# Performance work log

Hardware: AMD Instinct MI355X
Metric: run time of the kernel (lower is better)

Reference implementation:

```python
import jax, jax.numpy as jnp
import numpy as np

B, S, D, H = 128, 256, 256, 8   # graphs, nodes/graph, dim_h, heads
N = B * S
E = 524288
DH = D // H
BN_EPS = 1e-5

def _bn(v, g, b):
    # BatchNorm1d forward with batch statistics (biased var), eval-dropout model
    m = v.mean(0)
    var = v.var(0)
    return (v - m) * jax.lax.rsqrt(var + BN_EPS) * g + b

def setup_inputs() -> dict:
    key = jax.random.key(0)
    ks = jax.random.split(key, 40)
    x = jax.random.normal(ks[0], (N, D), jnp.float32)
    src = jax.random.randint(ks[1], (E,), 0, N)
    dst = (src // S) * S + jax.random.randint(ks[2], (E,), 0, S)  # intra-graph edges
    edge_index = jnp.stack([src, dst]).astype(jnp.int64)
    def lin(k, i, o):
        return (jax.random.normal(k, (i, o), jnp.float32) / np.float32(np.sqrt(i)))
    inp = {
        'x': x, 'edge_index': edge_index,
        'W_gcn': lin(ks[3], D, D), 'b_gcn': jnp.zeros((D,), jnp.float32),
        'W_gin1': lin(ks[4], D, D), 'b_gin1': jnp.zeros((D,), jnp.float32),
        'W_gin2': lin(ks[5], D, D), 'b_gin2': jnp.zeros((D,), jnp.float32),
        'g_kv': jnp.ones((D,), jnp.float32), 'be_kv': jnp.zeros((D,), jnp.float32),
        'Wq1': lin(ks[6], D, D), 'bq1': jnp.zeros((D,), jnp.float32),
        'Wq2': lin(ks[7], D, D), 'bq2': jnp.zeros((D,), jnp.float32),
        'Wq_a': lin(ks[8], D, D), 'bq_a': jnp.zeros((D,), jnp.float32),
        'Wk_a': lin(ks[9], D, D), 'bk_a': jnp.zeros((D,), jnp.float32),
        'Wv_a': lin(ks[10], D, D), 'bv_a': jnp.zeros((D,), jnp.float32),
        'Wo_a': lin(ks[11], D, D), 'bo_a': jnp.zeros((D,), jnp.float32),
        'g_attn': jnp.ones((D,), jnp.float32), 'be_attn': jnp.zeros((D,), jnp.float32),
        'Wf1': lin(ks[12], D, 2 * D), 'bf1': jnp.zeros((2 * D,), jnp.float32),
        'Wf2': lin(ks[13], 2 * D, D), 'bf2': jnp.zeros((D,), jnp.float32),
        'g2': jnp.ones((D,), jnp.float32), 'be2': jnp.zeros((D,), jnp.float32),
    }
    return inp

def _forward(x, edge_index,
             W_gcn, b_gcn, W_gin1, b_gin1, W_gin2, b_gin2, g_kv, be_kv,
             Wq1, bq1, Wq2, bq2,
             Wq_a, bq_a, Wk_a, bk_a, Wv_a, bv_a, Wo_a, bo_a, g_attn, be_attn,
             Wf1, bf1, Wf2, bf2, g2, be2):
    row, col = edge_index[0], edge_index[1]
    h_in1 = x

    # ---- expert 0: GCNConv (add self loops + symmetric norm) ----
    loops = jnp.arange(N, dtype=row.dtype)
    row2 = jnp.concatenate([row, loops])
    col2 = jnp.concatenate([col, loops])
    deg = jax.ops.segment_sum(jnp.ones_like(row2, jnp.float32), col2, num_segments=N)
    dinv = jnp.where(deg > 0, jax.lax.rsqrt(deg), 0.0)
    norm = dinv[row2] * dinv[col2]                     # [E+N]
    xw = x @ W_gcn                                      # [N, D]
    h_gcn = jax.ops.segment_sum(norm[:, None] * xw[row2], col2, num_segments=N) + b_gcn
    e0 = _bn(h_gcn, g_kv, be_kv)

    # ---- expert 1: GINConv (eps=0, sum aggregation, 2-layer MLP) ----
    agg = jax.ops.segment_sum(x[row], col, num_segments=N)
    h_gin = jax.nn.relu((x + agg) @ W_gin1 + b_gin1) @ W_gin2 + b_gin2
    e1 = _bn(h_gin, g_kv, be_kv)

    # ---- global expert normalization (torch .std -> unbiased) ----
    allo = jnp.concatenate([e0, e1], axis=0)
    gm = allo.mean()
    gs = jnp.std(allo, ddof=1)
    e0 = (e0 - gm) / (gs + 1e-8)
    e1 = (e1 - gm) / (gs + 1e-8)

    # ---- uniform routing & kv residual mix ----
    kv = 0.5 * e0 + 0.5 * e1 + 0.1 * h_in1              # [N, D]

    # ---- dense batching (equal-sized graphs -> pure reshape, full mask) ----
    q_dense = h_in1.reshape(B, S, D)
    kv_dense = kv.reshape(B, S, D)

    # ---- q projection MLP ----
    q_dense = jax.nn.relu(q_dense @ Wq1 + bq1) @ Wq2 + bq2

    # ---- multihead attention (batch_first, no padding) ----
    qh = (q_dense @ Wq_a + bq_a).reshape(B, S, H, DH)
    kh = (kv_dense @ Wk_a + bk_a).reshape(B, S, H, DH)
    vh = (kv_dense @ Wv_a + bv_a).reshape(B, S, H, DH)
    scores = jnp.einsum('bqhd,bkhd->bhqk', qh, kh) / np.float32(np.sqrt(DH))
    attn = jax.nn.softmax(scores, axis=-1)
    o = jnp.einsum('bhqk,bkhd->bqhd', attn, vh).reshape(B, S, D)
    h_attn = (o @ Wo_a + bo_a).reshape(N, D)

    # ---- residual + norm + FFN block ----
    h = _bn(h_in1 + h_attn, g_attn, be_attn)
    h_ff = jax.nn.relu(h @ Wf1 + bf1) @ Wf2 + bf2
    h = _bn(h + h_ff, g2, be2)
    return h

def reference(x, edge_index,
              W_gcn, b_gcn, W_gin1, b_gin1, W_gin2, b_gin2, g_kv, be_kv,
              Wq1, bq1, Wq2, bq2,
              Wq_a, bq_a, Wk_a, bk_a, Wv_a, bv_a, Wo_a, bo_a, g_attn, be_attn,
              Wf1, bf1, Wf2, bf2, g2, be2):
    return _forward(x, edge_index,
                    W_gcn, b_gcn, W_gin1, b_gin1, W_gin2, b_gin2, g_kv, be_kv,
                    Wq1, bq1, Wq2, bq2,
                    Wq_a, bq_a, Wk_a, bk_a, Wv_a, bv_a, Wo_a, bo_a, g_attn, be_attn,
                    Wf1, bf1, Wf2, bf2, g2, be2)
```

## Files before the change

kernel.cpp:

```cpp
#include <hip/hip_runtime.h>
#include <hip/hip_bf16.h>

typedef __hip_bfloat16 bf16;
typedef __attribute__((ext_vector_type(8))) short short8;
typedef __attribute__((ext_vector_type(4))) short short4v;
typedef __attribute__((ext_vector_type(4))) float f32x4;
typedef __attribute__((ext_vector_type(4))) int i32x4;

#define N_ 32768
#define D_ 256
#define S_ 256
#define B_ 128
#define E_ 524288

static __device__ __forceinline__ f32x4 mfma16(short8 a, short8 b, f32x4 c) {
  return __builtin_amdgcn_mfma_f32_16x16x32_bf16(a, b, c, 0, 0, 0);
}
static __device__ __forceinline__ f32x4 fzero4() {
  f32x4 z; z[0] = 0.f; z[1] = 0.f; z[2] = 0.f; z[3] = 0.f; return z;
}
static __device__ __forceinline__ float bits2f(short s) {
  unsigned u = ((unsigned)(unsigned short)s) << 16;
  return __builtin_bit_cast(float, u);
}
static __device__ __forceinline__ short f2bits(float f) {
  bf16 b = __float2bfloat16(f);
  return __builtin_bit_cast(short, b);
}
static __device__ __forceinline__ float tof(float x) { return x; }
static __device__ __forceinline__ float tof(bf16 x) { return __bfloat162float(x); }

#define GLOAD_LDS16(G, L) __builtin_amdgcn_global_load_lds( \
    (const __attribute__((address_space(1))) void*)(G),     \
    (__attribute__((address_space(3))) void*)(L), 16, 0, 0)

template<int F>
__global__ __launch_bounds__(256)
void gemm_bt(const bf16* __restrict__ A, const bf16* __restrict__ Bt,
             const float* __restrict__ bias, const void* __restrict__ resid,
             float* __restrict__ Cf, bf16* __restrict__ Cb,
             float* __restrict__ Sp, float* __restrict__ SSp,
             int M, int Nc, int K, long bsA, long bsB, long bsC)
{
  __shared__ __align__(16) bf16 lA[128 * 32];
  __shared__ __align__(16) bf16 lB[128 * 32];
  __shared__ float sS[2][128], sSS[2][128];
  const int z = blockIdx.z;
  const bf16* Ab = A + (long)z * bsA;
  const bf16* Bb = Bt + (long)z * bsB;
  const int m0 = blockIdx.x * 128, n0 = blockIdx.y * 128;
  const int tid = threadIdx.x;
  const int lane = tid & 63;
  const int w = tid >> 6, wr = w >> 1, wc = w & 1;
  const int g = lane >> 4, r = lane & 15, ko = g * 8;
  const int srow = lane >> 2, skw = (lane & 3) * 8;

  f32x4 acc[4][4];
  for (int i = 0; i < 4; i++) for (int j = 0; j < 4; j++) acc[i][j] = fzero4();

  for (int k0 = 0; k0 < K; k0 += 32) {
    __syncthreads();
    for (int i = 0; i < 2; i++) {
      const int c = w * 2 + i;
      GLOAD_LDS16(Ab + (long)(m0 + c * 16 + srow) * K + k0 + skw, lA + c * 512);
      GLOAD_LDS16(Bb + (long)(n0 + c * 16 + srow) * K + k0 + skw, lB + c * 512);
    }
    __syncthreads();
    short8 af[4], bfv[4];
    for (int mi = 0; mi < 4; mi++)
      af[mi] = *(const short8*)&lA[(wr * 64 + mi * 16 + r) * 32 + ko];
    for (int ni = 0; ni < 4; ni++)
      bfv[ni] = *(const short8*)&lB[(wc * 64 + ni * 16 + r) * 32 + ko];
    for (int mi = 0; mi < 4; mi++)
      for (int ni = 0; ni < 4; ni++)
        acc[mi][ni] = mfma16(af[mi], bfv[ni], acc[mi][ni]);
  }

  float cs[4] = {0, 0, 0, 0}, css[4] = {0, 0, 0, 0};
  for (int mi = 0; mi < 4; mi++) for (int ni = 0; ni < 4; ni++) {
    const int row = m0 + wr * 64 + mi * 16 + g * 4;
    const int col = n0 + wc * 64 + ni * 16 + r;
    float bv = (F & 2) ? bias[col] : 0.0f;
    for (int j = 0; j < 4; j++) {
      long idx = (long)(row + j) * Nc + col;
      float v = acc[mi][ni][j] + bv;
      if (F & 4)  v += ((const float*)resid)[(long)z * bsC + idx];
      if (F & 64) v += bits2f(((const short*)resid)[(long)z * bsC + idx]);
      if (F & 1)  v = fmaxf(v, 0.0f);
      if (F & 32) { cs[ni] += v; css[ni] += v * v; }
      if (F & 8)  Cf[(long)z * bsC + idx] = v;
      if (F & 16) Cb[(long)z * bsC + idx] = __float2bfloat16(v);
    }
  }
  if (F & 32) {
    for (int ni = 0; ni < 4; ni++) {
      cs[ni]  += __shfl_xor(cs[ni], 16);  cs[ni]  += __shfl_xor(cs[ni], 32);
      css[ni] += __shfl_xor(css[ni], 16); css[ni] += __shfl_xor(css[ni], 32);
    }
    if (lane < 16) {
      for (int ni = 0; ni < 4; ni++) {
        sS[wr][wc * 64 + ni * 16 + lane]  = cs[ni];
        sSS[wr][wc * 64 + ni * 16 + lane] = css[ni];
      }
    }
    __syncthreads();
    if (tid < 128) {
      atomicAdd(&Sp[n0 + tid],  sS[0][tid] + sS[1][tid]);
      atomicAdd(&SSp[n0 + tid], sSS[0][tid] + sSS[1][tid]);
    }
  }
}

__global__ __launch_bounds__(256, 2)
void attn_k(const bf16* __restrict__ qh, const bf16* __restrict__ kh,
            const bf16* __restrict__ vh, bf16* __restrict__ ob)
{
  const int h = blockIdx.x, b = blockIdx.y;
  const int tid = threadIdx.x, lane = tid & 63, w = tid >> 6;
  const int g = lane >> 4, r = lane & 15, ko = g * 8;
  __shared__ __align__(16) bf16 lK[256 * 32];
  __shared__ __align__(16) bf16 lV[32 * 256];
  char* lKc = (char*)lK;
  char* lVc = (char*)lV;

  for (int i = 0; i < 4; i++) {
    int c = tid + i * 256;
    int row = c >> 2, p4 = c & 3;
    short8 v = *(const short8*)(kh + (long)(b * 256 + row) * 256 + h * 32 + p4 * 8);
    *(short8*)(lKc + ((row * 64 + p4 * 16) ^ ((row & 7) << 4))) = v;
  }
  for (int i = 0; i < 4; i++) {
    int c = tid + i * 256;
    int s = c >> 2, part = c & 3;
    short8 v = *(const short8*)(vh + (long)(b * 256 + s) * 256 + h * 32 + part * 8);
    for (int j = 0; j < 8; j++) {
      int dh = part * 8 + j;
      int sw = ((dh & 7) ^ ((dh >> 3) << 1)) & 7;
      *(short*)(lVc + ((dh * 512 + s * 2) ^ (sw << 4))) = v[j];
    }
  }
  __syncthreads();

  const float scale = 0.17677669529663687f;
  const int idx0 = (((lane >> 4) & 1) * 32 + r) * 4;
  const int idx1 = idx0 + 64;
  const bool selhi = lane >= 32;

  for (int mc = 0; mc < 4; mc++) {
    const long qbase = (long)b * 256 + w * 64 + mc * 16;
    short8 qf = *(const short8*)(qh + (qbase + r) * 256 + h * 32 + ko);
    f32x4 sc[16];
    #pragma unroll
    for (int nc = 0; nc < 16; nc++) {
      int row = nc * 16 + r;
      short8 kf = *(const short8*)(lKc + ((row * 64 + g * 16) ^ ((r & 7) << 4)));
      sc[nc] = mfma16(kf, qf, fzero4());
    }
    f32x4 m4 = sc[0];
    #pragma unroll
    for (int nc = 1; nc < 16; nc++)
      for (int j = 0; j < 4; j++) m4[j] = fmaxf(m4[j], sc[nc][j]);
    float mx = fmaxf(fmaxf(m4[0], m4[1]), fmaxf(m4[2], m4[3]));
    mx = fmaxf(mx, __shfl_xor(mx, 16));
    mx = fmaxf(mx, __shfl_xor(mx, 32));
    f32x4 s4 = fzero4();
    #pragma unroll
    for (int nc = 0; nc < 16; nc++)
      for (int j = 0; j < 4; j++) {
        float p = __expf((sc[nc][j] - mx) * scale);
        sc[nc][j] = p; s4[j] += p;
      }
    float sum = s4[0] + s4[1] + s4[2] + s4[3];
    sum += __shfl_xor(sum, 16);
    sum += __shfl_xor(sum, 32);
    const float invs = 1.0f / sum;
    f32x4 oa[2]; oa[0] = fzero4(); oa[1] = fzero4();
    #pragma unroll
    for (int kc = 0; kc < 8; kc++) {
      int pkA0, pkA1, pkB0, pkB1;
      {
        const f32x4 pa = sc[2 * kc], pb = sc[2 * kc + 1];
        unsigned a0 = (unsigned short)f2bits(pa[0] * invs);
        unsigned a1 = (unsigned short)f2bits(pa[1] * invs);
        unsigned a2 = (unsigned short)f2bits(pa[2] * invs);
        unsigned a3 = (unsigned short)f2bits(pa[3] * invs);
        unsigned b0 = (unsigned short)f2bits(pb[0] * invs);
        unsigned b1 = (unsigned short)f2bits(pb[1] * invs);
        unsigned b2 = (unsigned short)f2bits(pb[2] * invs);
        unsigned b3 = (unsigned short)f2bits(pb[3] * invs);
        pkA0 = (int)((a1 << 16) | a0);
        pkA1 = (int)((a3 << 16) | a2);
        pkB0 = (int)((b1 << 16) | b0);
        pkB1 = (int)((b3 << 16) | b2);
      }
      int A0 = __builtin_amdgcn_ds_bpermute(idx0, pkA0);
      int A1 = __builtin_amdgcn_ds_bpermute(idx0, pkA1);
      int B0 = __builtin_amdgcn_ds_bpermute(idx0, pkB0);
      int B1 = __builtin_amdgcn_ds_bpermute(idx0, pkB1);
      int C0 = __builtin_amdgcn_ds_bpermute(idx1, pkA0);
      int C1 = __builtin_amdgcn_ds_bpermute(idx1, pkA1);
      int D0 = __builtin_amdgcn_ds_bpermute(idx1, pkB0);
      int D1 = __builtin_amdgcn_ds_bpermute(idx1, pkB1);
      i32x4 av;
      av[0] = selhi ? B0 : A0;
      av[1] = selhi ? B1 : A1;
      av[2] = selhi ? D0 : C0;
      av[3] = selhi ? D1 : C1;
      short8 af = __builtin_bit_cast(short8, av);
      #pragma unroll
      for (int n = 0; n < 2; n++) {
        int dh = n * 16 + r;
        int sw = ((dh & 7) ^ ((dh >> 3) << 1)) & 7;
        short8 bv = *(const short8*)(lVc + ((dh * 512 + kc * 64 + g * 16) ^ (sw << 4)));
        oa[n] = mfma16(af, bv, oa[n]);
      }
    }
    #pragma unroll
    for (int n = 0; n < 2; n++)
      for (int j = 0; j < 4; j++)
        ob[(qbase + g * 4 + j) * 256 + h * 32 + n * 16 + r] =
          __float2bfloat16(oa[n][j]);
  }
}

template<typename TIN>
__global__ __launch_bounds__(256)
void transpose_cast_k(const TIN* __restrict__ in, bf16* __restrict__ out,
                      int in_rs, int out_rs, long zhi, long out_zs)
{
  __shared__ float tile[32][33];
  const int z = blockIdx.z;
  const long ioff = (long)z * zhi;
  const long ooff = (long)z * out_zs;
  const int tx = threadIdx.x, ty = threadIdx.y;
  const int c = blockIdx.x * 32 + tx;
  const int rb = blockIdx.y * 32;
  for (int i = 0; i < 4; i++)
    tile[ty + i * 8][tx] = tof(in[ioff + (long)(rb + ty + i * 8) * in_rs + c]);
  __syncthreads();
  const int oc = rb + tx;
  const int orb = blockIdx.x * 32;
  for (int i = 0; i < 4; i++)
    out[ooff + (long)(orb + ty + i * 8) * out_rs + oc] =
      __float2bfloat16(tile[tx][ty + i * 8]);
}

__global__ __launch_bounds__(256)
void w9t_k(const float* w0, const float* w1, const float* w2, const float* w3,
           const float* w4, const float* w5, const float* w6, const float* w7,
           const float* w8, bf16* __restrict__ out)
{
  __shared__ float tile[32][33];
  const float* srcs[9] = {w0, w1, w2, w3, w4, w5, w6, w7, w8};
  const int wi = blockIdx.z;
  const float* in = srcs[wi];
  bf16* o = out + (long)wi * 65536;
  const int tx = threadIdx.x, ty = threadIdx.y;
  const int c = blockIdx.x * 32 + tx;
  const int rb = blockIdx.y * 32;
  for (int i = 0; i < 4; i++)
    tile[ty + i * 8][tx] = in[(rb + ty + i * 8) * 256 + c];
  __syncthreads();
  const int oc = rb + tx;
  const int orb = blockIdx.x * 32;
  for (int i = 0; i < 4; i++)
    o[(orb + ty + i * 8) * 256 + oc] = __float2bfloat16(tile[tx][ty + i * 8]);
}

__global__ __launch_bounds__(256)
void cast4_k(const float* __restrict__ in, bf16* __restrict__ out)
{
  long i = ((long)blockIdx.x * 256 + threadIdx.x) * 4;
  float4 v = *(const float4*)(in + i);
  short4v o;
  o[0] = f2bits(v.x); o[1] = f2bits(v.y); o[2] = f2bits(v.z); o[3] = f2bits(v.w);
  *(short4v*)(out + i) = o;
}

__global__ __launch_bounds__(256)
void edge_cnt_k(const int* __restrict__ ei, unsigned* __restrict__ cnt)
{
  int e = blockIdx.x * 256 + threadIdx.x;
  int src = ei[e], dst = ei[E_ + e];
  long idx = ((long)(src >> 8) * 256 + (dst & 255)) * 256 + (src & 255);
  atomicAdd(&cnt[idx >> 1], 1u << ((idx & 1) * 16));
}

__global__ __launch_bounds__(256)
void deg_k(const unsigned* __restrict__ cnt, float* __restrict__ dinv)
{
  int rid = blockIdx.x * 16 + (threadIdx.x >> 4);
  int l16 = threadIdx.x & 15;
  const uint4* rp = (const uint4*)(cnt + (long)rid * 128);
  unsigned s = 0;
  for (int i = 0; i < 2; i++) {
    uint4 v = rp[l16 + i * 16];
    s += (v.x & 0xFFFF) + (v.x >> 16) + (v.y & 0xFFFF) + (v.y >> 16)
       + (v.z & 0xFFFF) + (v.z >> 16) + (v.w & 0xFFFF) + (v.w >> 16);
  }
  s += __shfl_xor(s, 1); s += __shfl_xor(s, 2);
  s += __shfl_xor(s, 4); s += __shfl_xor(s, 8);
  if (l16 == 0) dinv[rid] = rsqrtf((float)s + 1.0f);
}

__global__ __launch_bounds__(256)
void adj_derive_k(const unsigned* __restrict__ cnt, const float* __restrict__ dinv,
                  bf16* __restrict__ gin, bf16* __restrict__ gcn)
{
  long i = ((long)blockIdx.x * 256 + threadIdx.x) * 4;
  uint2 cp = *(const uint2*)(cnt + (i >> 1));
  float cv[4] = {(float)(cp.x & 0xFFFF), (float)(cp.x >> 16),
                 (float)(cp.y & 0xFFFF), (float)(cp.y >> 16)};
  long row = i >> 8;
  int g = (int)(row >> 8), dst = (int)(row & 255);
  int src0 = (int)(i & 255);
  float dd = dinv[row];
  const float* ds = dinv + (long)g * 256 + src0;
  short4v oi, oc;
  for (int j = 0; j < 4; j++) {
    float gv = cv[j] * dd * ds[j];
    if (src0 + j == dst) gv += dd * dd;
    oi[j] = f2bits(cv[j]);
    oc[j] = f2bits(gv);
  }
  *(short4v*)(gin + i) = oi;
  *(short4v*)(gcn + i) = oc;
}

__global__ __launch_bounds__(256)
void expert_stats_k(const float* __restrict__ S0, const float* __restrict__ SS0,
                    const float* __restrict__ S1, const float* __restrict__ SS1,
                    const float* __restrict__ gkv, const float* __restrict__ bkv,
                    float* __restrict__ kA, float* __restrict__ kB,
                    float* __restrict__ kC)
{
  const int d = threadIdx.x;
  const float invN = 1.0f / 32768.0f;
  float m0 = S0[d] * invN, v0 = SS0[d] * invN - m0 * m0;
  float a0 = gkv[d] * rsqrtf(v0 + 1e-5f), c0 = bkv[d] - m0 * a0;
  float m1 = S1[d] * invN, v1 = SS1[d] * invN - m1 * m1;
  float a1 = gkv[d] * rsqrtf(v1 + 1e-5f), c1 = bkv[d] - m1 * a1;
  float gsum = a0 * S0[d] + 32768.0f * c0 + a1 * S1[d] + 32768.0f * c1;
  float gss  = a0 * a0 * SS0[d] + 2.0f * a0 * c0 * S0[d] + 32768.0f * c0 * c0
             + a1 * a1 * SS1[d] + 2.0f * a1 * c1 * S1[d] + 32768.0f * c1 * c1;
  __shared__ float r1[256], r2[256];
  r1[d] = gsum; r2[d] = gss;
  __syncthreads();
  for (int s = 128; s > 0; s >>= 1) {
    if (d < s) { r1[d] += r1[d + s]; r2[d] += r2[d + s]; }
    __syncthreads();
  }
  const float cntall = 16777216.0f;
  float tg = r1[0], tss = r2[0];
  float gm = tg / cntall;
  float var = (tss - tg * tg / cntall) / (cntall - 1.0f);
  float gs = sqrtf(fmaxf(var, 0.f)) + 1e-8f;
  kA[d] = 0.5f * a0 / gs;
  kB[d] = 0.5f * a1 / gs;
  kC[d] = 0.5f * (c0 + c1 - 2.0f * gm) / gs;
}

__global__ __launch_bounds__(256)
void kv_mix_k(const bf16* __restrict__ hgcn, const bf16* __restrict__ hgin,
              const bf16* __restrict__ xb, const float* __restrict__ kA,
              const float* __restrict__ kB, const float* __restrict__ kC,
              bf16* __restrict__ kv)
{
  long i = ((long)blockIdx.x * 256 + threadIdx.x) * 8;
  int d0 = (int)(i & 255);
  short8 a = *(const short8*)(hgcn + i);
  short8 b = *(const short8*)(hgin + i);
  short8 c = *(const short8*)(xb + i);
  short8 o;
  for (int j = 0; j < 8; j++) {
    int d = d0 + j;
    float v = kA[d] * bits2f(a[j]) + kB[d] * bits2f(b[j]) + kC[d] + 0.1f * bits2f(c[j]);
    o[j] = f2bits(v);
  }
  *(short8*)(kv + i) = o;
}

template<int MODE>
__global__ __launch_bounds__(256)
void bn_apply_k(const bf16* __restrict__ in, const float* __restrict__ S,
                const float* __restrict__ SSq, const float* __restrict__ gg,
                const float* __restrict__ bb, float* __restrict__ outf,
                bf16* __restrict__ outb)
{
  long i = ((long)blockIdx.x * 256 + threadIdx.x) * 8;
  int d0 = (int)(i & 255);
  short8 v = *(const short8*)(in + i);
  const float invN = 1.0f / 32768.0f;
  float4 o0, o1; short8 o8;
  for (int j = 0; j < 8; j++) {
    int d = d0 + j;
    float m = S[d] * invN;
    float var = SSq[d] * invN - m * m;
    float a = gg[d] * rsqrtf(var + 1e-5f);
    float c = bb[d] - m * a;
    float o = a * bits2f(v[j]) + c;
    if (MODE & 1) { if (j < 4) (&o0.x)[j] = o; else (&o1.x)[j - 4] = o; }
    if (MODE & 2) o8[j] = f2bits(o);
  }
  if (MODE & 1) { *(float4*)(outf + i) = o0; *(float4*)(outf + i + 4) = o1; }
  if (MODE & 2) *(short8*)(outb + i) = o8;
}

static constexpr size_t OFF_S0 = 0, OFF_SS0 = 1024, OFF_S1 = 2048, OFF_SS1 = 3072;
static constexpr size_t OFF_S2 = 4096, OFF_SS2 = 5120, OFF_S3 = 6144, OFF_SS3 = 7168;
static constexpr size_t OFF_KA = 8192, OFF_KB = 9216, OFF_KC = 10240;
static constexpr size_t OFF_CNT = 16384;
static constexpr size_t CNT_BYTES = (size_t)B_ * S_ * S_ * 2;
static constexpr size_t ZERO_BYTES = OFF_CNT + CNT_BYTES;
static constexpr size_t OFF_DINV = ZERO_BYTES;
static constexpr size_t OFF_W = OFF_DINV + 131072;
static constexpr size_t NDB2 = (size_t)N_ * D_ * 2;
static constexpr size_t OFF_ADJGINB = OFF_W + 1703936;
static constexpr size_t OFF_ADJGCNB = OFF_ADJGINB + NDB2;
static constexpr size_t OFF_XB   = OFF_ADJGCNB + NDB2;
static constexpr size_t OFF_XT   = OFF_XB + NDB2;
static constexpr size_t OFF_AGG  = OFF_XT + NDB2;
static constexpr size_t OFF_GIN  = OFF_AGG + NDB2;
static constexpr size_t OFF_KV   = OFF_GIN + NDB2;
static constexpr size_t OFF_HGCN = OFF_KV + NDB2;
static constexpr size_t OFF_HGIN = OFF_HGCN + NDB2;

extern "C" void kernel_launch(void* const* d_in, const int* in_sizes, int n_in,
                              void* d_out, int out_size, void* d_ws, size_t ws_size,
                              hipStream_t stream)
{
  (void)in_sizes; (void)n_in; (void)out_size; (void)ws_size;
  const float* x      = (const float*)d_in[0];
  const int*   ei     = (const int*)d_in[1];
  const float* W_gcn  = (const float*)d_in[2];
  const float* b_gcn  = (const float*)d_in[3];
  const float* W_gin1 = (const float*)d_in[4];
  const float* b_gin1 = (const float*)d_in[5];
  const float* W_gin2 = (const float*)d_in[6];
  const float* b_gin2 = (const float*)d_in[7];
  const float* g_kv   = (const float*)d_in[8];
  const float* be_kv  = (const float*)d_in[9];
  const float* Wq1    = (const float*)d_in[10];
  const float* bq1    = (const float*)d_in[11];
  const float* Wq2    = (const float*)d_in[12];
  const float* bq2    = (const float*)d_in[13];
  const float* Wq_a   = (const float*)d_in[14];
  const float* bq_a   = (const float*)d_in[15];
  const float* Wk_a   = (const float*)d_in[16];
  const float* bk_a   = (const float*)d_in[17];
  const float* Wv_a   = (const float*)d_in[18];
  const float* bv_a   = (const float*)d_in[19];
  const float* Wo_a   = (const float*)d_in[20];
  const float* bo_a   = (const float*)d_in[21];
  const float* g_attn = (const float*)d_in[22];
  const float* be_attn= (const float*)d_in[23];
  const float* Wf1    = (const float*)d_in[24];
  const float* bf1    = (const float*)d_in[25];
  const float* Wf2    = (const float*)d_in[26];
  const float* bf2    = (const float*)d_in[27];
  const float* g2     = (const float*)d_in[28];
  const float* be2    = (const float*)d_in[29];

  char* ws = (char*)d_ws;
  float* S0  = (float*)(ws + OFF_S0);  float* SS0 = (float*)(ws + OFF_SS0);
  float* S1  = (float*)(ws + OFF_S1);  float* SS1 = (float*)(ws + OFF_SS1);
  float* S2  = (float*)(ws + OFF_S2);  float* SS2 = (float*)(ws + OFF_SS2);
  float* S3  = (float*)(ws + OFF_S3);  float* SS3 = (float*)(ws + OFF_SS3);
  float* kA  = (float*)(ws + OFF_KA);  float* kB  = (float*)(ws + OFF_KB);
  float* kC  = (float*)(ws + OFF_KC);
  unsigned* cntA = (unsigned*)(ws + OFF_CNT);
  float* dinv = (float*)(ws + OFF_DINV);
  bf16* wT = (bf16*)(ws + OFF_W);
  bf16 *WgcnT = wT,            *Wgin1T = wT + 65536,  *Wgin2T = wT + 131072;
  bf16 *Wq1T  = wT + 196608,   *Wq2T   = wT + 262144, *WqaT   = wT + 327680;
  bf16 *WkaT  = wT + 393216,   *WvaT   = wT + 458752, *WoaT   = wT + 524288;
  bf16 *Wf1T  = wT + 589824,   *Wf2T   = wT + 720896;
  bf16* adjGINb = (bf16*)(ws + OFF_ADJGINB);
  bf16* adjGCNb = (bf16*)(ws + OFF_ADJGCNB);
  bf16* xb    = (bf16*)(ws + OFF_XB);
  bf16* xT    = (bf16*)(ws + OFF_XT);
  bf16* aggb  = (bf16*)(ws + OFF_AGG);
  bf16* gin_in= (bf16*)(ws + OFF_GIN);
  bf16* kv_bf = (bf16*)(ws + OFF_KV);
  bf16* hgcnb = (bf16*)(ws + OFF_HGCN);
  bf16* hginb = (bf16*)(ws + OFF_HGIN);
  bf16* gin_h  = adjGCNb;
  bf16* qhb    = adjGINb;
  bf16* q1b    = xT;
  bf16* qb     = aggb;
  bf16* khb    = gin_in;
  bf16* vhb    = hgcnb;
  bf16* ob     = hginb;
  bf16* tbufb  = (bf16*)(ws + OFF_CNT);
  bf16* hb     = xb;
  bf16* f1b    = adjGINb;
  bf16* t2b    = gin_in;
  float* outp  = (float*)d_out;

  hipMemsetAsync(d_ws, 0, ZERO_BYTES, stream);

  dim3 tb(32, 8);
  w9t_k<<<dim3(8, 8, 9), tb, 0, stream>>>(W_gcn, W_gin1, W_gin2, Wq1, Wq2,
                                          Wq_a, Wk_a, Wv_a, Wo_a, wT);
  transpose_cast_k<float><<<dim3(16, 8, 1), tb, 0, stream>>>(Wf1, Wf1T, 512, 256, 0, 0);
  transpose_cast_k<float><<<dim3(8, 16, 1), tb, 0, stream>>>(Wf2, Wf2T, 256, 512, 0, 0);
  cast4_k<<<8192, 256, 0, stream>>>(x, xb);
  transpose_cast_k<float><<<dim3(8, 8, 128), tb, 0, stream>>>(x, xT, 256, 256, 65536, 65536);
  edge_cnt_k<<<2048, 256, 0, stream>>>(ei, cntA);
  deg_k<<<2048, 256, 0, stream>>>(cntA, dinv);
  adj_derive_k<<<8192, 256, 0, stream>>>(cntA, dinv, adjGINb, adjGCNb);
  gemm_bt<16><<<dim3(2, 2, 128), 256, 0, stream>>>(adjGCNb, xT, nullptr, nullptr,
      nullptr, aggb, nullptr, nullptr, 256, 256, 256, 65536, 65536, 65536);
  gemm_bt<80><<<dim3(2, 2, 128), 256, 0, stream>>>(adjGINb, xT, nullptr, xb,
      nullptr, gin_in, nullptr, nullptr, 256, 256, 256, 65536, 65536, 65536);
  gemm_bt<50><<<dim3(256, 2, 1), 256, 0, stream>>>(aggb, WgcnT, b_gcn, nullptr,
      nullptr, hgcnb, S0, SS0, N_, 256, 256, 0, 0, 0);
  gemm_bt<19><<<dim3(256, 2, 1), 256, 0, stream>>>(gin_in, Wgin1T, b_gin1, nullptr,
      nullptr, gin_h, nullptr, nullptr, N_, 256, 256, 0, 0, 0);
  gemm_bt<50><<<dim3(256, 2, 1), 256, 0, stream>>>(gin_h, Wgin2T, b_gin2, nullptr,
      nullptr, hginb, S1, SS1, N_, 256, 256, 0, 0, 0);
  expert_stats_k<<<1, 256, 0, stream>>>(S0, SS0, S1, SS1, g_kv, be_kv, kA, kB, kC);
  kv_mix_k<<<4096, 256, 0, stream>>>(hgcnb, hginb, xb, kA, kB, kC, kv_bf);
  gemm_bt<19><<<dim3(256, 2, 1), 256, 0, stream>>>(xb, Wq1T, bq1, nullptr,
      nullptr, q1b, nullptr, nullptr, N_, 256, 256, 0, 0, 0);
  gemm_bt<18><<<dim3(256, 2, 1), 256, 0, stream>>>(q1b, Wq2T, bq2, nullptr,
      nullptr, qb, nullptr, nullptr, N_, 256, 256, 0, 0, 0);
  gemm_bt<18><<<dim3(256, 2, 1), 256, 0, stream>>>(qb, WqaT, bq_a, nullptr,
      nullptr, qhb, nullptr, nullptr, N_, 256, 256, 0, 0, 0);
  gemm_bt<18><<<dim3(256, 2, 1), 256, 0, stream>>>(kv_bf, WkaT, bk_a, nullptr,
      nullptr, khb, nullptr, nullptr, N_, 256, 256, 0, 0, 0);
  gemm_bt<18><<<dim3(256, 2, 1), 256, 0, stream>>>(kv_bf, WvaT, bv_a, nullptr,
      nullptr, vhb, nullptr, nullptr, N_, 256, 256, 0, 0, 0);
  attn_k<<<dim3(8, 128), 256, 0, stream>>>(qhb, khb, vhb, ob);
  gemm_bt<114><<<dim3(256, 2, 1), 256, 0, stream>>>(ob, WoaT, bo_a, xb,
      nullptr, tbufb, S2, SS2, N_, 256, 256, 0, 0, 0);
  bn_apply_k<2><<<4096, 256, 0, stream>>>(tbufb, S2, SS2, g_attn, be_attn, nullptr, hb);
  gemm_bt<19><<<dim3(256, 4, 1), 256, 0, stream>>>(hb, Wf1T, bf1, nullptr,
      nullptr, f1b, nullptr, nullptr, N_, 512, 256, 0, 0, 0);
  gemm_bt<114><<<dim3(256, 2, 1), 256, 0, stream>>>(f1b, Wf2T, bf2, hb,
      nullptr, t2b, S3, SS3, N_, 256, 512, 0, 0, 0);
  bn_apply_k<1><<<4096, 256, 0, stream>>>(t2b, S3, SS3, g2, be2, outp, nullptr);
}
```

Measured before the change: 342.9 us.

## Fuse chained GIN and query linear layers into LDS-resident MLP kernel, merge K/V GEMM

Adds a kernel that runs 2 or 3 chained 256x256 linear layers per 64-row tile, keeping intermediate activations in swizzled LDS. It replaces the separate GIN two-layer GEMMs and the three-stage query projection chain, removing intermediate global writes and reads and several launches. The K and V projections become one 512-wide GEMM with a second bias pointer, and the attention kernel reads them with a 512 stride. It also raises wave priority around the attention MFMA loops. The cost is that the fused kernel reloads full weight tiles per block with a simple, unpipelined K loop and has smaller per-wave tiles.

```diff
diff --git a/kernel.cpp b/kernel.cpp
--- a/kernel.cpp
+++ b/kernel.cpp
@@ -37,7 +37,8 @@
 template<int F>
 __global__ __launch_bounds__(256)
 void gemm_bt(const bf16* __restrict__ A, const bf16* __restrict__ Bt,
-             const float* __restrict__ bias, const void* __restrict__ resid,
+             const float* __restrict__ bias, const float* __restrict__ biasB,
+             const void* __restrict__ resid,
              float* __restrict__ Cf, bf16* __restrict__ Cb,
              float* __restrict__ Sp, float* __restrict__ SSp,
              int M, int Nc, int K, long bsA, long bsB, long bsC)
@@ -80,7 +81,11 @@
   for (int mi = 0; mi < 4; mi++) for (int ni = 0; ni < 4; ni++) {
     const int row = m0 + wr * 64 + mi * 16 + g * 4;
     const int col = n0 + wc * 64 + ni * 16 + r;
-    float bv = (F & 2) ? bias[col] : 0.0f;
+    float bv = 0.0f;
+    if (F & 2) {
+      if ((F & 128) && col >= 256) bv = biasB[col - 256];
+      else bv = bias[col];
+    }
     for (int j = 0; j < 4; j++) {
       long idx = (long)(row + j) * Nc + col;
       float v = acc[mi][ni][j] + bv;
@@ -111,9 +116,132 @@
   }
 }
 
+template<int STAGES, bool STATS>
+__global__ __launch_bounds__(512)
+void mlp_fused(const bf16* __restrict__ A,
+               const bf16* __restrict__ B1, const float* __restrict__ b1,
+               const bf16* __restrict__ B2, const float* __restrict__ b2,
+               const bf16* __restrict__ B3, const float* __restrict__ b3,
+               bf16* __restrict__ C, float* __restrict__ Sp, float* __restrict__ SSp)
+{
+  __shared__ __align__(16) bf16 lA[64 * 32];
+  __shared__ __align__(16) bf16 lB[256 * 32];
+  __shared__ __align__(16) bf16 lC[64 * 256];
+  char* lCc = (char*)lC;
+  const int tid = threadIdx.x;
+  const int lane = tid & 63;
+  const int w = tid >> 6;
+  const int mh = w >> 2, nq = w & 3;
+  const int g = lane >> 4, r = lane & 15, ko = g * 8;
+  const int m0 = blockIdx.x * 64;
+
+  f32x4 acc[2][4];
+  for (int i = 0; i < 2; i++) for (int j = 0; j < 4; j++) acc[i][j] = fzero4();
+
+  for (int k0 = 0; k0 < 256; k0 += 32) {
+    __syncthreads();
+    if (tid < 256)
+      GLOAD_LDS16(A + (long)(m0 + (tid >> 2)) * 256 + k0 + (tid & 3) * 8,
+                  lA + w * 512);
+    GLOAD_LDS16(B1 + (long)(tid >> 2) * 256 + k0 + (tid & 3) * 8,
+                lB + w * 512);
+    GLOAD_LDS16(B1 + (long)((tid + 512) >> 2) * 256 + k0 + ((tid + 512) & 3) * 8,
+                lB + w * 512 + 4096);
+    __syncthreads();
+    short8 af[2], bfv[4];
+    for (int mi = 0; mi < 2; mi++)
+      af[mi] = *(const short8*)&lA[(mh * 32 + mi * 16 + r) * 32 + ko];
+    for (int ni = 0; ni < 4; ni++)
+      bfv[ni] = *(const short8*)&lB[(nq * 64 + ni * 16 + r) * 32 + ko];
+    for (int mi = 0; mi < 2; mi++)
+      for (int ni = 0; ni < 4; ni++)
+        acc[mi][ni] = mfma16(af[mi], bfv[ni], acc[mi][ni]);
+  }
+  for (int mi = 0; mi < 2; mi++) for (int ni = 0; ni < 4; ni++) {
+    const int col = nq * 64 + ni * 16 + r;
+    const float bv = b1[col];
+    for (int j = 0; j < 4; j++) {
+      const int row = mh * 32 + mi * 16 + g * 4 + j;
+      float v = fmaxf(acc[mi][ni][j] + bv, 0.0f);
+      *(short*)(lCc + ((row * 512 + col * 2) ^ ((row & 7) << 4))) = f2bits(v);
+    }
+  }
+  __syncthreads();
+
+  const bf16* Bs = B2;
+  for (int s = 1; s < STAGES; s++) {
+    for (int i = 0; i < 2; i++) for (int j = 0; j < 4; j++) acc[i][j] = fzero4();
+    for (int k0 = 0; k0 < 256; k0 += 32) {
+      __syncthreads();
+      GLOAD_LDS16(Bs + (long)(tid >> 2) * 256 + k0 + (tid & 3) * 8,
+                  lB + w * 512);
+      GLOAD_LDS16(Bs + (long)((tid + 512) >> 2) * 256 + k0 + ((tid + 512) & 3) * 8,
+                  lB + w * 512 + 4096);
+      __syncthreads();
+      short8 af[2], bfv[4];
+      for (int mi = 0; mi < 2; mi++) {
+        const int row = mh * 32 + mi * 16 + r;
+        af[mi] = *(const short8*)(lCc +
+                  ((row * 512 + (k0 + ko) * 2) ^ ((row & 7) << 4)));
+      }
+      for (int ni = 0; ni < 4; ni++)
+        bfv[ni] = *(const short8*)&lB[(nq * 64 + ni * 16 + r) * 32 + ko];
+      for (int mi = 0; mi < 2; mi++)
+        for (int ni = 0; ni < 4; ni++)
+          acc[mi][ni] = mfma16(af[mi], bfv[ni], acc[mi][ni]);
+    }
+    if (s < STAGES - 1) {
+      __syncthreads();
+      for (int mi = 0; mi < 2; mi++) for (int ni = 0; ni < 4; ni++) {
+        const int col = nq * 64 + ni * 16 + r;
+        const float bv = b2[col];
+        for (int j = 0; j < 4; j++) {
+          const int row = mh * 32 + mi * 16 + g * 4 + j;
+          float v = acc[mi][ni][j] + bv;
+          *(short*)(lCc + ((row * 512 + col * 2) ^ ((row & 7) << 4))) = f2bits(v);
+        }
+      }
+      __syncthreads();
+      Bs = B3;
+    }
+  }
+
+  const float* bf_ = (STAGES == 3) ? b3 : b2;
+  float cs[4] = {0, 0, 0, 0}, css[4] = {0, 0, 0, 0};
+  for (int mi = 0; mi < 2; mi++) for (int ni = 0; ni < 4; ni++) {
+    const int col = nq * 64 + ni * 16 + r;
+    const float bv = bf_[col];
+    for (int j = 0; j < 4; j++) {
+      const int row = mh * 32 + mi * 16 + g * 4 + j;
+      float v = acc[mi][ni][j] + bv;
+      if (STATS) { cs[ni] += v; css[ni] += v * v; }
+      C[(long)(m0 + row) * 256 + col] = __float2bfloat16(v);
+    }
+  }
+  if (STATS) {
+    for (int ni = 0; ni < 4; ni++) {
+      cs[ni]  += __shfl_xor(cs[ni], 16);  cs[ni]  += __shfl_xor(cs[ni], 32);
+      css[ni] += __shfl_xor(css[ni], 16); css[ni] += __shfl_xor(css[ni], 32);
+    }
+    __syncthreads();
+    float* sS = (float*)lC;
+    if (lane < 16) {
+      for (int ni = 0; ni < 4; ni++) {
+        sS[mh * 256 + nq * 64 + ni * 16 + lane] = cs[ni];
+        sS[512 + mh * 256 + nq * 64 + ni * 16 + lane] = css[ni];
+      }
+    }
+    __syncthreads();
+    if (tid < 256) {
+      atomicAdd(&Sp[tid],  sS[tid] + sS[256 + tid]);
+      atomicAdd(&SSp[tid], sS[512 + tid] + sS[768 + tid]);
+    }
+  }
+}
+
 __global__ __launch_bounds__(256, 2)
 void attn_k(const bf16* __restrict__ qh, const bf16* __restrict__ kh,
-            const bf16* __restrict__ vh, bf16* __restrict__ ob)
+            const bf16* __restrict__ vh, bf16* __restrict__ ob, int ks)
 {
   const int h = blockIdx.x, b = blockIdx.y;
   const int tid = threadIdx.x, lane = tid & 63, w = tid >> 6;
@@ -126,13 +254,13 @@
   for (int i = 0; i < 4; i++) {
     int c = tid + i * 256;
     int row = c >> 2, p4 = c & 3;
-    short8 v = *(const short8*)(kh + (long)(b * 256 + row) * 256 + h * 32 + p4 * 8);
+    short8 v = *(const short8*)(kh + (long)(b * 256 + row) * ks + h * 32 + p4 * 8);
     *(short8*)(lKc + ((row * 64 + p4 * 16) ^ ((row & 7) << 4))) = v;
   }
   for (int i = 0; i < 4; i++) {
     int c = tid + i * 256;
     int s = c >> 2, part = c & 3;
-    short8 v = *(const short8*)(vh + (long)(b * 256 + s) * 256 + h * 32 + part * 8);
+    short8 v = *(const short8*)(vh + (long)(b * 256 + s) * ks + h * 32 + part * 8);
     for (int j = 0; j < 8; j++) {
       int dh = part * 8 + j;
       int sw = ((dh & 7) ^ ((dh >> 3) << 1)) & 7;
@@ -150,12 +278,14 @@
     const long qbase = (long)b * 256 + w * 64 + mc * 16;
     short8 qf = *(const short8*)(qh + (qbase + r) * 256 + h * 32 + ko);
     f32x4 sc[16];
+    __builtin_amdgcn_s_setprio(1);
     #pragma unroll
     for (int nc = 0; nc < 16; nc++) {
       int row = nc * 16 + r;
       short8 kf = *(const short8*)(lKc + ((row * 64 + g * 16) ^ ((r & 7) << 4)));
       sc[nc] = mfma16(kf, qf, fzero4());
     }
+    __builtin_amdgcn_s_setprio(0);
     f32x4 m4 = sc[0];
     #pragma unroll
     for (int nc = 1; nc < 16; nc++)
@@ -175,6 +305,7 @@
     sum += __shfl_xor(sum, 32);
     const float invs = 1.0f / sum;
     f32x4 oa[2]; oa[0] = fzero4(); oa[1] = fzero4();
+    __builtin_amdgcn_s_setprio(1);
     #pragma unroll
     for (int kc = 0; kc < 8; kc++) {
       int pkA0, pkA1, pkB0, pkB1;
@@ -215,6 +346,7 @@
         oa[n] = mfma16(af, bv, oa[n]);
       }
     }
+    __builtin_amdgcn_s_setprio(0);
     #pragma unroll
     for (int n = 0; n < 2; n++)
       for (int j = 0; j < 4; j++)
@@ -475,6 +607,7 @@
   bf16 *Wq1T  = wT + 196608,   *Wq2T   = wT + 262144, *WqaT   = wT + 327680;
   bf16 *WkaT  = wT + 393216,   *WvaT   = wT + 458752, *WoaT   = wT + 524288;
   bf16 *Wf1T  = wT + 589824,   *Wf2T   = wT + 720896;
+  (void)WvaT;
   bf16* adjGINb = (bf16*)(ws + OFF_ADJGINB);
   bf16* adjGCNb = (bf16*)(ws + OFF_ADJGCNB);
   bf16* xb    = (bf16*)(ws + OFF_XB);
@@ -484,17 +617,13 @@
   bf16* kv_bf = (bf16*)(ws + OFF_KV);
   bf16* hgcnb = (bf16*)(ws + OFF_HGCN);
   bf16* hginb = (bf16*)(ws + OFF_HGIN);
-  bf16* gin_h  = adjGCNb;
   bf16* qhb    = adjGINb;
-  bf16* q1b    = xT;
-  bf16* qb     = aggb;
-  bf16* khb    = gin_in;
-  bf16* vhb    = hgcnb;
+  bf16* khvb   = aggb;
   bf16* ob     = hginb;
   bf16* tbufb  = (bf16*)(ws + OFF_CNT);
   bf16* hb     = xb;
   bf16* f1b    = adjGINb;
-  bf16* t2b    = gin_in;
+  bf16* t2b    = (bf16*)(ws + OFF_CNT);
   float* outp  = (float*)d_out;
 
   hipMemsetAsync(d_ws, 0, ZERO_BYTES, stream);
@@ -510,34 +639,26 @@
   deg_k<<<2048, 256, 0, stream>>>(cntA, dinv);
   adj_derive_k<<<8192, 256, 0, stream>>>(cntA, dinv, adjGINb, adjGCNb);
   gemm_bt<16><<<dim3(2, 2, 128), 256, 0, stream>>>(adjGCNb, xT, nullptr, nullptr,
-      nullptr, aggb, nullptr, nullptr, 256, 256, 256, 65536, 65536, 65536);
-  gemm_bt<80><<<dim3(2, 2, 128), 256, 0, stream>>>(adjGINb, xT, nullptr, xb,
-      nullptr, gin_in, nullptr, nullptr, 256, 256, 256, 65536, 65536, 65536);
+      nullptr, nullptr, aggb, nullptr, nullptr, 256, 256, 256, 65536, 65536, 65536);
+  gemm_bt<80><<<dim3(2, 2, 128), 256, 0, stream>>>(adjGINb, xT, nullptr, nullptr,
+      xb, nullptr, gin_in, nullptr, nullptr, 256, 256, 256, 65536, 65536, 65536);
   gemm_bt<50><<<dim3(256, 2, 1), 256, 0, stream>>>(aggb, WgcnT, b_gcn, nullptr,
-      nullptr, hgcnb, S0, SS0, N_, 256, 256, 0, 0, 0);
-  gemm_bt<19><<<dim3(256, 2, 1), 256, 0, stream>>>(gin_in, Wgin1T, b_gin1, nullptr,
-      nullptr, gin_h, nullptr, nullptr, N_, 256, 256, 0, 0, 0);
-  gemm_bt<50><<<dim3(256, 2, 1), 256, 0, stream>>>(gin_h, Wgin2T, b_gin2, nullptr,
-      nullptr, hginb, S1, SS1, N_, 256, 256, 0, 0, 0);
+      nullptr, nullptr, hgcnb, S0, SS0, N_, 256, 256, 0, 0, 0);
+  mlp_fused<2, true><<<512, 512, 0, stream>>>(gin_in, Wgin1T, b_gin1,
+      Wgin2T, b_gin2, nullptr, nullptr, hginb, S1, SS1);
   expert_stats_k<<<1, 256, 0, stream>>>(S0, SS0, S1, SS1, g_kv, be_kv, kA, kB, kC);
   kv_mix_k<<<4096, 256, 0, stream>>>(hgcnb, hginb, xb, kA, kB, kC, kv_bf);
-  gemm_bt<19><<<dim3(256, 2, 1), 256, 0, stream>>>(xb, Wq1T, bq1, nullptr,
-      nullptr, q1b, nullptr, nullptr, N_, 256, 256, 0, 0, 0);
-  gemm_bt<18><<<dim3(256, 2, 1), 256, 0, stream>>>(q1b, Wq2T, bq2, nullptr,
-      nullptr, qb, nullptr, nullptr, N_, 256, 256, 0, 0, 0);
-  gemm_bt<18><<<dim3(256, 2, 1), 256, 0, stream>>>(qb, WqaT, bq_a, nullptr,
-      nullptr, qhb, nullptr, nullptr, N_, 256, 256, 0, 0, 0);
-  gemm_bt<18><<<dim3(256, 2, 1), 256, 0, stream>>>(kv_bf, WkaT, bk_a, nullptr,
-      nullptr, khb, nullptr, nullptr, N_, 256, 256, 0, 0, 0);
-  gemm_bt<18><<<dim3(256, 2, 1), 256, 0, stream>>>(kv_bf, WvaT, bv_a, nullptr,
-      nullptr, vhb, nullptr, nullptr, N_, 256, 256, 0, 0, 0);
-  attn_k<<<dim3(8, 128), 256, 0, stream>>>(qhb, khb, vhb, ob);
-  gemm_bt<114><<<dim3(256, 2, 1), 256, 0, stream>>>(ob, WoaT, bo_a, xb,
-      nullptr, tbufb, S2, SS2, N_, 256, 256, 0, 0, 0);
+  mlp_fused<3, false><<<512, 512, 0, stream>>>(xb, Wq1T, bq1,
+      Wq2T, bq2, WqaT, bq_a, qhb, nullptr, nullptr);
+  gemm_bt<146><<<dim3(256, 4, 1), 256, 0, stream>>>(kv_bf, WkaT, bk_a, bv_a,
+      nullptr, nullptr, khvb, nullptr, nullptr, N_, 512, 256, 0, 0, 0);
+  attn_k<<<dim3(8, 128), 256, 0, stream>>>(qhb, khvb, khvb + 256, ob, 512);
+  gemm_bt<114><<<dim3(256, 2, 1), 256, 0, stream>>>(ob, WoaT, bo_a, nullptr,
+      xb, nullptr, tbufb, S2, SS2, N_, 256, 256, 0, 0, 0);
   bn_apply_k<2><<<4096, 256, 0, stream>>>(tbufb, S2, SS2, g_attn, be_attn, nullptr, hb);
   gemm_bt<19><<<dim3(256, 4, 1), 256, 0, stream>>>(hb, Wf1T, bf1, nullptr,
-      nullptr, f1b, nullptr, nullptr, N_, 512, 256, 0, 0, 0);
-  gemm_bt<114><<<dim3(256, 2, 1), 256, 0, stream>>>(f1b, Wf2T, bf2, hb,
-      nullptr, t2b, S3, SS3, N_, 256, 512, 0, 0, 0);
+      nullptr, nullptr, f1b, nullptr, nullptr, N_, 512, 256, 0, 0, 0);
+  gemm_bt<114><<<dim3(256, 2, 1), 256, 0, stream>>>(f1b, Wf2T, bf2, nullptr,
+      hb, nullptr, t2b, S3, SS3, N_, 256, 512, 0, 0, 0);
   bn_apply_k<1><<<4096, 256, 0, stream>>>(t2b, S3, SS3, g2, be2, outp, nullptr);
 }
```

Result: faster. 331.1 us (-3.5%).
